# Kernel optimization log

Measured on AMD Instinct MI355X. Metric: run time of the kernel, lower is better.

## Reference

```python
import jax, jax.numpy as jnp
import numpy as np

N = 10000
E = 160000
EMB = 10
ITERS = 3


def _linear_params(key, fan_in, fan_out):
    kw, kb = jax.random.split(key)
    # xavier-normal-ish init for the weight, small uniform for bias (as torch Linear default scale)
    w = jax.random.normal(kw, (fan_in, fan_out), dtype=jnp.float32) * np.float32(np.sqrt(2.0 / (fan_in + fan_out)))
    b = jax.random.uniform(kb, (fan_out,), dtype=jnp.float32, minval=-0.1, maxval=0.1)
    return w, b


def setup_inputs() -> dict:
    key = jax.random.key(0)
    ks = jax.random.split(key, 10)
    features = jax.random.normal(ks[0], (N,), dtype=jnp.float32)
    weights = jax.random.uniform(ks[1], (E,), dtype=jnp.float32)
    adjacency = jax.random.uniform(ks[2], (N, N), dtype=jnp.float32)
    ws_w, ws_b = _linear_params(ks[3], 1, EMB)          # w_selected
    wnp_w, wnp_b = _linear_params(ks[4], EMB, EMB)      # w_nbpriors
    wnw_w, wnw_b = _linear_params(ks[5], EMB, EMB)      # w_nbweights
    wew_w, wew_b = _linear_params(ks[6], 1, EMB)        # w_nbweights_ew
    wqr_w, wqr_b = _linear_params(ks[7], 2 * EMB, 1)    # w_q_reduc
    wqa_w, wqa_b = _linear_params(ks[8], EMB, EMB)      # w_q_allembed
    wqact_w, wqact_b = _linear_params(ks[9], EMB, EMB)  # w_q_action
    return {
        "features": features, "weights": weights, "adjacency": adjacency,
        "ws_w": ws_w, "ws_b": ws_b,
        "wnp_w": wnp_w, "wnp_b": wnp_b,
        "wnw_w": wnw_w, "wnw_b": wnw_b,
        "wew_w": wew_w, "wew_b": wew_b,
        "wqr_w": wqr_w, "wqr_b": wqr_b,
        "wqa_w": wqa_w, "wqa_b": wqa_b,
        "wqact_w": wqact_w, "wqact_b": wqact_b,
    }


def reference(features, weights, adjacency,
              ws_w, ws_b, wnp_w, wnp_b, wnw_w, wnw_b, wew_w, wew_b,
              wqr_w, wqr_b, wqa_w, wqa_b, wqact_w, wqact_b):
    n = adjacency.shape[0]
    # v_selected = w_selected(features[:, None])  -> (N, EMB)
    v_selected = features[:, None] @ ws_w + ws_b
    # edge weight embedding, summed over edges -> single (EMB,) vector
    edge_emb = jax.nn.relu(weights[:, None] @ wew_w + wew_b)  # (E, EMB)
    v_weights = jnp.sum(edge_emb, axis=0) @ wnw_w + wnw_b     # (EMB,)

    embeddings = jnp.zeros((n, EMB), dtype=features.dtype)
    for _ in range(ITERS):  # small fixed iteration count
        v_priors = (adjacency @ embeddings) @ wnp_w + wnp_b   # (N, EMB)
        embeddings = jax.nn.relu(v_selected + v_weights + v_priors)

    sumembed = jnp.sum(embeddings, axis=0) @ wqa_w + wqa_b    # (EMB,)
    peract = embeddings @ wqact_w + wqact_b                   # (N, EMB)
    q_in = jnp.concatenate([jnp.broadcast_to(sumembed[None, :], (n, EMB)), peract], axis=1)
    q_vals = (q_in @ wqr_w + wqr_b)[:, 0]                     # (N,)
    return q_vals, embeddings
```

## Files before the change

### kernel.cpp

```cpp
#include <hip/hip_runtime.h>

#define N_NODES 10000
#define EMB 10
#define NCHUNK 2500
#define ROWS 4

typedef float f32x4 __attribute__((ext_vector_type(4)));

#define WS_SEDGE 0
#define WS_SSUM  16
#define WS_EMBT  64

__global__ void k_edge_sum(const float* __restrict__ w, int E,
                           const float* __restrict__ wew_w,
                           const float* __restrict__ wew_b,
                           float* __restrict__ sEdge) {
    __shared__ float red[4][EMB];
    float a[EMB], b[EMB], acc[EMB];
#pragma unroll
    for (int j = 0; j < EMB; ++j) { a[j] = wew_w[j]; b[j] = wew_b[j]; acc[j] = 0.f; }
    for (int e = blockIdx.x * blockDim.x + threadIdx.x; e < E; e += gridDim.x * blockDim.x) {
        float we = w[e];
#pragma unroll
        for (int j = 0; j < EMB; ++j) acc[j] += fmaxf(we * a[j] + b[j], 0.f);
    }
#pragma unroll
    for (int m = 1; m < 64; m <<= 1)
#pragma unroll
        for (int j = 0; j < EMB; ++j) acc[j] += __shfl_xor(acc[j], m, 64);
    int wave = threadIdx.x >> 6, lane = threadIdx.x & 63;
    if (lane == 0)
#pragma unroll
        for (int j = 0; j < EMB; ++j) red[wave][j] = acc[j];
    __syncthreads();
    if (threadIdx.x < EMB)
        atomicAdd(&sEdge[threadIdx.x],
                  red[0][threadIdx.x] + red[1][threadIdx.x] + red[2][threadIdx.x] + red[3][threadIdx.x]);
}

template <bool FIRST>
__global__ __launch_bounds__(256) void k_iter(
    const float* __restrict__ A, const float* __restrict__ embT_in,
    const float* __restrict__ f, const float* __restrict__ ws_w,
    const float* __restrict__ ws_b, const float* __restrict__ wnp_w,
    const float* __restrict__ wnp_b, const float* __restrict__ wnw_w,
    const float* __restrict__ wnw_b, const float* __restrict__ sEdge,
    const float* __restrict__ wqr_w, const float* __restrict__ wqact_w,
    float* __restrict__ embT_out, float* __restrict__ emb_out,
    float* __restrict__ ssum, float* __restrict__ q_out) {
    const int tid  = threadIdx.x;
    const int wave = tid >> 6;
    const int lane = tid & 63;
    const int r0   = blockIdx.x * ROWS;

    __shared__ float s_cb2[EMB];
    __shared__ float s_qvec[EMB];
    if (tid < EMB) {
        int j = tid;
        float v = wnw_b[j];
#pragma unroll
        for (int k = 0; k < EMB; ++k) v += sEdge[k] * wnw_w[k * EMB + j];
        s_cb2[j] = v + ws_b[j] + wnp_b[j];
        if (!FIRST) {
            float qv = 0.f;
#pragma unroll
            for (int k = 0; k < EMB; ++k) qv += wqact_w[j * EMB + k] * wqr_w[EMB + k];
            s_qvec[j] = qv;
        }
    }
    __syncthreads();
    float cb2[EMB], wsw[EMB];
#pragma unroll
    for (int j = 0; j < EMB; ++j) { cb2[j] = s_cb2[j]; wsw[j] = ws_w[j]; }

    float acc[ROWS][EMB] = {};

    const f32x4* A0 = (const f32x4*)(A + (size_t)(r0 + 0) * N_NODES);
    const f32x4* A1 = (const f32x4*)(A + (size_t)(r0 + 1) * N_NODES);
    const f32x4* A2 = (const f32x4*)(A + (size_t)(r0 + 2) * N_NODES);
    const f32x4* A3 = (const f32x4*)(A + (size_t)(r0 + 3) * N_NODES);
    const f32x4* F4 = (const f32x4*)f;

#define BODY(c)                                                                     \
    {                                                                               \
        f32x4 a0 = A0[c], a1 = A1[c], a2 = A2[c], a3 = A3[c];                       \
        f32x4 f4;                                                                   \
        if (FIRST) f4 = F4[c];                                                      \
        _Pragma("unroll")                                                           \
        for (int j = 0; j < EMB; ++j) {                                             \
            f32x4 e;                                                                \
            if (FIRST) {                                                            \
                e.x = fmaxf(f4.x * wsw[j] + cb2[j], 0.f);                           \
                e.y = fmaxf(f4.y * wsw[j] + cb2[j], 0.f);                           \
                e.z = fmaxf(f4.z * wsw[j] + cb2[j], 0.f);                           \
                e.w = fmaxf(f4.w * wsw[j] + cb2[j], 0.f);                           \
            } else {                                                                \
                e = ((const f32x4*)(embT_in + (size_t)j * N_NODES))[c];             \
            }                                                                       \
            acc[0][j] += a0.x * e.x + a0.y * e.y + a0.z * e.z + a0.w * e.w;         \
            acc[1][j] += a1.x * e.x + a1.y * e.y + a1.z * e.z + a1.w * e.w;         \
            acc[2][j] += a2.x * e.x + a2.y * e.y + a2.z * e.z + a2.w * e.w;         \
            acc[3][j] += a3.x * e.x + a3.y * e.y + a3.z * e.z + a3.w * e.w;         \
        }                                                                           \
    }

    if (!FIRST) {
        if (tid < NCHUNK - 9 * 256) { int c = 9 * 256 + tid; BODY(c) }
    }
#pragma unroll 1
    for (int s = 0; s < 9; ++s) {
        int c = (FIRST ? s : (8 - s)) * 256 + tid;
        BODY(c)
    }
    if (FIRST) {
        if (tid < NCHUNK - 9 * 256) { int c = 9 * 256 + tid; BODY(c) }
    }
#undef BODY

#pragma unroll
    for (int m = 1; m < 64; m <<= 1)
#pragma unroll
        for (int r = 0; r < ROWS; ++r)
#pragma unroll
            for (int j = 0; j < EMB; ++j) acc[r][j] += __shfl_xor(acc[r][j], m, 64);

    __shared__ float part[4][ROWS * EMB];
    __shared__ float colp[ROWS * EMB];
    if (lane == 0)
#pragma unroll
        for (int r = 0; r < ROWS; ++r)
#pragma unroll
            for (int j = 0; j < EMB; ++j) part[wave][r * EMB + j] = acc[r][j];
    __syncthreads();

    if (tid < ROWS * EMB) {
        int r = tid / EMB, j = tid % EMB;
        float v = 0.f;
#pragma unroll
        for (int k = 0; k < EMB; ++k) {
            float yk = part[0][r * EMB + k] + part[1][r * EMB + k] +
                       part[2][r * EMB + k] + part[3][r * EMB + k];
            v += yk * wnp_w[k * EMB + j];
        }
        int i = r0 + r;
        v = fmaxf(f[i] * wsw[j] + cb2[j] + v, 0.f);
        if (FIRST) {
            embT_out[(size_t)j * N_NODES + i] = v;
        } else {
            emb_out[(size_t)i * EMB + j] = v;
            colp[tid] = v;
        }
    }
    if (!FIRST) {
        __syncthreads();
        if (tid < EMB)
            atomicAdd(&ssum[tid],
                      colp[tid] + colp[EMB + tid] + colp[2 * EMB + tid] + colp[3 * EMB + tid]);
        if (tid < ROWS) {
            float q = 0.f;
#pragma unroll
            for (int j = 0; j < EMB; ++j) q += colp[tid * EMB + j] * s_qvec[j];
            q_out[r0 + tid] = q;
        }
    }
}

__global__ void k_qc(const float* __restrict__ ssum,
                     const float* __restrict__ wqa_w, const float* __restrict__ wqa_b,
                     const float* __restrict__ wqr_w, const float* __restrict__ wqr_b,
                     const float* __restrict__ wqact_b,
                     float* __restrict__ q_out) {
    __shared__ float s_qc;
    if (threadIdx.x == 0) {
        float qc = wqr_b[0];
        for (int t = 0; t < EMB; ++t) {
            float se = wqa_b[t];
            for (int k = 0; k < EMB; ++k) se += ssum[k] * wqa_w[k * EMB + t];
            qc += se * wqr_w[t] + wqact_b[t] * wqr_w[EMB + t];
        }
        s_qc = qc;
    }
    __syncthreads();
    int i = blockIdx.x * blockDim.x + threadIdx.x;
    if (i < N_NODES) q_out[i] += s_qc;
}

extern "C" void kernel_launch(void* const* d_in, const int* in_sizes, int n_in,
                              void* d_out, int out_size, void* d_ws, size_t ws_size,
                              hipStream_t stream) {
    (void)n_in; (void)out_size; (void)ws_size;
    const float* f      = (const float*)d_in[0];
    const float* w      = (const float*)d_in[1];
    const float* A      = (const float*)d_in[2];
    const float* ws_w   = (const float*)d_in[3];
    const float* ws_b   = (const float*)d_in[4];
    const float* wnp_w  = (const float*)d_in[5];
    const float* wnp_b  = (const float*)d_in[6];
    const float* wnw_w  = (const float*)d_in[7];
    const float* wnw_b  = (const float*)d_in[8];
    const float* wew_w  = (const float*)d_in[9];
    const float* wew_b  = (const float*)d_in[10];
    const float* wqr_w  = (const float*)d_in[11];
    const float* wqr_b  = (const float*)d_in[12];
    const float* wqa_w  = (const float*)d_in[13];
    const float* wqa_b  = (const float*)d_in[14];
    const float* wqact_w = (const float*)d_in[15];
    const float* wqact_b = (const float*)d_in[16];
    float* ws  = (float*)d_ws;
    float* out = (float*)d_out;
    const int E = in_sizes[1];

    float* outEmb = out + N_NODES;

    hipMemsetAsync(ws, 0, 64 * sizeof(float), stream);
    k_edge_sum<<<256, 256, 0, stream>>>(w, E, wew_w, wew_b, ws + WS_SEDGE);
    k_iter<true><<<N_NODES / ROWS, 256, 0, stream>>>(
        A, nullptr, f, ws_w, ws_b, wnp_w, wnp_b, wnw_w, wnw_b, ws + WS_SEDGE,
        nullptr, nullptr, ws + WS_EMBT, nullptr, nullptr, nullptr);
    k_iter<false><<<N_NODES / ROWS, 256, 0, stream>>>(
        A, ws + WS_EMBT, f, ws_w, ws_b, wnp_w, wnp_b, wnw_w, wnw_b, ws + WS_SEDGE,
        wqr_w, wqact_w, nullptr, outEmb, ws + WS_SSUM, out);
    k_qc<<<(N_NODES + 255) / 256, 256, 0, stream>>>(ws + WS_SSUM, wqa_w, wqa_b,
                                                    wqr_w, wqr_b, wqact_b, out);
}
```

Baseline: 682.6 us.

## Process two row groups per block and batch column-sum atomics

Each block of k_iter now handles two groups of four adjacency rows in sequence, so the grid is halved, and launch bounds request at least 5 blocks per SIMD. Column sums are gathered in shared memory and written with one atomic per column per block, halving global atomics. The reverse-order chunk traversal in the second pass is dropped, which removes the L2 reuse of the embedding chunks last touched by the previous pass. The occupancy hint may cap registers and cause spills given the large accumulator arrays.

```diff
diff --git a/kernel.cpp b/kernel.cpp
--- a/kernel.cpp
+++ b/kernel.cpp
@@ -4,6 +4,8 @@
 #define EMB 10
 #define NCHUNK 2500
 #define ROWS 4
+#define GROUPS 2
+#define NBLK2 1250
 
 typedef float f32x4 __attribute__((ext_vector_type(4)));
 
@@ -39,7 +41,7 @@
 }
 
 template <bool FIRST>
-__global__ __launch_bounds__(256) void k_iter(
+__global__ __launch_bounds__(256, 5) void k_iter(
     const float* __restrict__ A, const float* __restrict__ embT_in,
     const float* __restrict__ f, const float* __restrict__ ws_w,
     const float* __restrict__ ws_b, const float* __restrict__ wnp_w,
@@ -51,10 +53,12 @@
     const int tid  = threadIdx.x;
     const int wave = tid >> 6;
     const int lane = tid & 63;
-    const int r0   = blockIdx.x * ROWS;
 
     __shared__ float s_cb2[EMB];
     __shared__ float s_qvec[EMB];
+    __shared__ float part_l[4][ROWS * EMB];
+    __shared__ float colp[ROWS * EMB];
+    __shared__ float s_colsum[EMB];
     if (tid < EMB) {
         int j = tid;
         float v = wnw_b[j];
@@ -67,19 +71,22 @@
             for (int k = 0; k < EMB; ++k) qv += wqact_w[j * EMB + k] * wqr_w[EMB + k];
             s_qvec[j] = qv;
         }
+        s_colsum[j] = 0.f;
     }
     __syncthreads();
     float cb2[EMB], wsw[EMB];
 #pragma unroll
     for (int j = 0; j < EMB; ++j) { cb2[j] = s_cb2[j]; wsw[j] = ws_w[j]; }
 
-    float acc[ROWS][EMB] = {};
-
-    const f32x4* A0 = (const f32x4*)(A + (size_t)(r0 + 0) * N_NODES);
-    const f32x4* A1 = (const f32x4*)(A + (size_t)(r0 + 1) * N_NODES);
-    const f32x4* A2 = (const f32x4*)(A + (size_t)(r0 + 2) * N_NODES);
-    const f32x4* A3 = (const f32x4*)(A + (size_t)(r0 + 3) * N_NODES);
-    const f32x4* F4 = (const f32x4*)f;
+#pragma unroll 1
+    for (int g = 0; g < GROUPS; ++g) {
+        const int r0 = (blockIdx.x + g * NBLK2) * ROWS;
+        float acc[ROWS][EMB] = {};
+        const f32x4* A0 = (const f32x4*)(A + (size_t)(r0 + 0) * N_NODES);
+        const f32x4* A1 = (const f32x4*)(A + (size_t)(r0 + 1) * N_NODES);
+        const f32x4* A2 = (const f32x4*)(A + (size_t)(r0 + 2) * N_NODES);
+        const f32x4* A3 = (const f32x4*)(A + (size_t)(r0 + 3) * N_NODES);
+        const f32x4* F4 = (const f32x4*)f;
 
 #define BODY(c)                                                                     \
     {                                                                               \
@@ -104,64 +111,60 @@
         }                                                                           \
     }
 
+#pragma unroll 1
+        for (int s = 0; s < 9; ++s) { int c = s * 256 + tid; BODY(c) }
+        if (tid < NCHUNK - 9 * 256) { int c = 9 * 256 + tid; BODY(c) }
+#undef BODY
+
+#pragma unroll
+        for (int m = 1; m < 64; m <<= 1)
+#pragma unroll
+            for (int r = 0; r < ROWS; ++r)
+#pragma unroll
+                for (int j = 0; j < EMB; ++j) acc[r][j] += __shfl_xor(acc[r][j], m, 64);
+
+        __syncthreads();
+        if (lane == 0)
+#pragma unroll
+            for (int r = 0; r < ROWS; ++r)
+#pragma unroll
+                for (int j = 0; j < EMB; ++j) part_l[wave][r * EMB + j] = acc[r][j];
+        __syncthreads();
+
+        if (tid < ROWS * EMB) {
+            int r = tid / EMB, j = tid % EMB;
+            float v = 0.f;
+#pragma unroll
+            for (int k = 0; k < EMB; ++k) {
+                float yk = part_l[0][r * EMB + k] + part_l[1][r * EMB + k] +
+                           part_l[2][r * EMB + k] + part_l[3][r * EMB + k];
+                v += yk * wnp_w[k * EMB + j];
+            }
+            int i = r0 + r;
+            v = fmaxf(f[i] * wsw[j] + cb2[j] + v, 0.f);
+            if (FIRST) {
+                embT_out[(size_t)j * N_NODES + i] = v;
+            } else {
+                emb_out[(size_t)i * EMB + j] = v;
+                colp[tid] = v;
+            }
+        }
+        if (!FIRST) {
+            __syncthreads();
+            if (tid < EMB)
+                s_colsum[tid] += colp[tid] + colp[EMB + tid] +
+                                 colp[2 * EMB + tid] + colp[3 * EMB + tid];
+            if (tid < ROWS) {
+                float q = 0.f;
+#pragma unroll
+                for (int j = 0; j < EMB; ++j) q += colp[tid * EMB + j] * s_qvec[j];
+                q_out[r0 + tid] = q;
+            }
+        }
+    }
     if (!FIRST) {
-        if (tid < NCHUNK - 9 * 256) { int c = 9 * 256 + tid; BODY(c) }
-    }
-#pragma unroll 1
-    for (int s = 0; s < 9; ++s) {
-        int c = (FIRST ? s : (8 - s)) * 256 + tid;
-        BODY(c)
-    }
-    if (FIRST) {
-        if (tid < NCHUNK - 9 * 256) { int c = 9 * 256 + tid; BODY(c) }
-    }
-#undef BODY
-
-#pragma unroll
-    for (int m = 1; m < 64; m <<= 1)
-#pragma unroll
-        for (int r = 0; r < ROWS; ++r)
-#pragma unroll
-            for (int j = 0; j < EMB; ++j) acc[r][j] += __shfl_xor(acc[r][j], m, 64);
-
-    __shared__ float part[4][ROWS * EMB];
-    __shared__ float colp[ROWS * EMB];
-    if (lane == 0)
-#pragma unroll
-        for (int r = 0; r < ROWS; ++r)
-#pragma unroll
-            for (int j = 0; j < EMB; ++j) part[wave][r * EMB + j] = acc[r][j];
-    __syncthreads();
-
-    if (tid < ROWS * EMB) {
-        int r = tid / EMB, j = tid % EMB;
-        float v = 0.f;
-#pragma unroll
-        for (int k = 0; k < EMB; ++k) {
-            float yk = part[0][r * EMB + k] + part[1][r * EMB + k] +
-                       part[2][r * EMB + k] + part[3][r * EMB + k];
-            v += yk * wnp_w[k * EMB + j];
-        }
-        int i = r0 + r;
-        v = fmaxf(f[i] * wsw[j] + cb2[j] + v, 0.f);
-        if (FIRST) {
-            embT_out[(size_t)j * N_NODES + i] = v;
-        } else {
-            emb_out[(size_t)i * EMB + j] = v;
-            colp[tid] = v;
-        }
-    }
-    if (!FIRST) {
-        __syncthreads();
         if (tid < EMB)
-            atomicAdd(&ssum[tid],
-                      colp[tid] + colp[EMB + tid] + colp[2 * EMB + tid] + colp[3 * EMB + tid]);
-        if (tid < ROWS) {
-            float q = 0.f;
-#pragma unroll
-            for (int j = 0; j < EMB; ++j) q += colp[tid * EMB + j] * s_qvec[j];
-            q_out[r0 + tid] = q;
-        }
+            atomicAdd(&ssum[tid], s_colsum[tid]);
     }
 }
 
@@ -214,10 +217,10 @@
 
     hipMemsetAsync(ws, 0, 64 * sizeof(float), stream);
     k_edge_sum<<<256, 256, 0, stream>>>(w, E, wew_w, wew_b, ws + WS_SEDGE);
-    k_iter<true><<<N_NODES / ROWS, 256, 0, stream>>>(
+    k_iter<true><<<NBLK2, 256, 0, stream>>>(
         A, nullptr, f, ws_w, ws_b, wnp_w, wnp_b, wnw_w, wnw_b, ws + WS_SEDGE,
         nullptr, nullptr, ws + WS_EMBT, nullptr, nullptr, nullptr);
-    k_iter<false><<<N_NODES / ROWS, 256, 0, stream>>>(
+    k_iter<false><<<NBLK2, 256, 0, stream>>>(
         A, ws + WS_EMBT, f, ws_w, ws_b, wnp_w, wnp_b, wnw_w, wnw_b, ws + WS_SEDGE,
         wqr_w, wqact_w, nullptr, outEmb, ws + WS_SSUM, out);
     k_qc<<<(N_NODES + 255) / 256, 256, 0, stream>>>(ws + WS_SSUM, wqa_w, wqa_b,
```

Result: slower. 720.0 us (+5.5%).
